# Performance work log

Hardware: AMD Instinct MI355X
Metric: run time of the kernel (lower is better)

Reference implementation:

```python
import jax, jax.numpy as jnp
import numpy as np

LMAX, MMAX = 4, 2
C = 128          # sphere_channels
MOUT = 128       # m_output_channels
N = 32768        # number of edges
K = sum(2 * min(l, MMAX) + 1 for l in range(LMAX + 1))  # 19 coefficients
LN_EPS = 1e-5


def build_to_m():
    # l-major ordering of (l, m) coefficients -> m-major permutation matrix
    ms = np.array([m for l in range(LMAX + 1)
                   for m in range(-min(l, MMAX), min(l, MMAX) + 1)])
    order = list(np.nonzero(ms == 0)[0])
    for m in range(1, MMAX + 1):
        order += list(np.nonzero(ms == m)[0]) + list(np.nonzero(ms == -m)[0])
    P = np.zeros((K, K), np.float32)
    P[np.arange(K), order] = 1.0
    return jnp.asarray(P)


TO_M = build_to_m()
M_SIZE = [LMAX + 1] + [LMAX - m + 1 for m in range(1, MMAX + 1)]  # [5, 4, 3]


def _layernorm(h, g, b):
    mu = jnp.mean(h, axis=-1, keepdims=True)
    var = jnp.mean(jnp.square(h - mu), axis=-1, keepdims=True)
    return (h - mu) * jax.lax.rsqrt(var + LN_EPS) * g + b


def _radial_mlp(x, w1, b1, g1, be1, w2, b2, g2, be2, w3, b3):
    h = jax.nn.silu(_layernorm(x @ w1.T + b1, g1, be1))
    h = jax.nn.silu(_layernorm(h @ w2.T + b2, g2, be2))
    return h @ w3.T + b3  # [N, 1536]


def setup_inputs() -> dict:
    key = jax.random.key(0)
    ks = jax.random.split(key, 16)
    s = 0.02
    return {
        "x": jax.random.normal(ks[0], (N, K, C), jnp.float32),
        "x_edge": jax.random.normal(ks[1], (N, C), jnp.float32),
        "fc0_w": jax.random.normal(ks[2], (MOUT * 5, 5 * C), jnp.float32) * s,
        "fc0_b": jax.random.normal(ks[3], (MOUT * 5,), jnp.float32) * s,
        "fc1_w": jax.random.normal(ks[4], (MOUT * 4, 4 * C), jnp.float32) * s,
        "fc2_w": jax.random.normal(ks[5], (MOUT * 3, 3 * C), jnp.float32) * s,
        "rad_w1": jax.random.normal(ks[6], (C, C), jnp.float32) * s,
        "rad_b1": jax.random.normal(ks[7], (C,), jnp.float32) * s,
        "rad_g1": jnp.ones((C,), jnp.float32),
        "rad_beta1": jnp.zeros((C,), jnp.float32),
        "rad_w2": jax.random.normal(ks[8], (C, C), jnp.float32) * s,
        "rad_b2": jax.random.normal(ks[9], (C,), jnp.float32) * s,
        "rad_g2": jnp.ones((C,), jnp.float32),
        "rad_beta2": jnp.zeros((C,), jnp.float32),
        "rad_w3": jax.random.normal(ks[10], (1536, C), jnp.float32) * s,
        "rad_b3": jax.random.normal(ks[11], (1536,), jnp.float32) * s,
    }


def reference(x, x_edge, fc0_w, fc0_b, fc1_w, fc2_w,
              rad_w1, rad_b1, rad_g1, rad_beta1,
              rad_w2, rad_b2, rad_g2, rad_beta2,
              rad_w3, rad_b3):
    n = x.shape[0]
    # reorder coefficients by m (to_m is a permutation)
    xm = jnp.einsum('nac,ba->nbc', x, TO_M)
    rad = _radial_mlp(x_edge, rad_w1, rad_b1, rad_g1, rad_beta1,
                      rad_w2, rad_b2, rad_g2, rad_beta2, rad_w3, rad_b3)

    # m = 0 block
    sz0 = M_SIZE[0]
    x0 = xm[:, :sz0].reshape(n, sz0 * C) * rad[:, :sz0 * C]
    y0 = (x0 @ fc0_w.T + fc0_b).reshape(n, sz0, MOUT)
    outs = [y0]

    offset, offr = sz0, sz0 * C
    for m, fcw in zip((1, 2), (fc1_w, fc2_w)):
        sz = M_SIZE[m]
        din = sz * C
        xb = xm[:, offset:offset + 2 * sz].reshape(n, 2, din)
        xb = xb * rad[:, offr:offr + din][:, None, :]  # FiLM radial scale
        yb = (xb @ fcw.T).reshape(n, 2 * sz, MOUT)
        outs.append(yb)
        offset += 2 * sz
        offr += din

    out = jnp.concatenate(outs, axis=1)  # [N, K, MOUT]
    # project back from m-major ordering
    return jnp.einsum('nac,ab->nbc', out, TO_M)
```

## Files before the change

### kernel.cpp

```cpp
#include <hip/hip_runtime.h>

typedef __bf16 bf16x8 __attribute__((ext_vector_type(8)));
typedef __bf16 bf16x4 __attribute__((ext_vector_type(4)));
typedef float f32x4 __attribute__((ext_vector_type(4)));

#define MFMA_16x16x32_BF16(a, b, c) __builtin_amdgcn_mfma_f32_16x16x32_bf16(a, b, c, 0, 0, 0)

typedef const __attribute__((address_space(1))) unsigned int* gas_ptr;
typedef __attribute__((address_space(3))) unsigned int* las_ptr;

__device__ __forceinline__ void gload_lds16(const void* g, void* l) {
    __builtin_amdgcn_global_load_lds((gas_ptr)(unsigned long long)g,
                                     (las_ptr)(unsigned long long)l, 16, 0, 0);
}

__constant__ int ORDER_C[19] = {0, 2, 6, 11, 16, 3, 7, 12, 17, 1, 5, 10, 15, 8, 13, 18, 4, 9, 14};

__global__ __launch_bounds__(256) void wconv_kernel(
    const float* __restrict__ fc0, const float* __restrict__ fc1,
    const float* __restrict__ fc2, const float* __restrict__ rw1,
    const float* __restrict__ rw2, const float* __restrict__ rw3,
    __bf16* __restrict__ o) {
    int i4 = (blockIdx.x * 256 + threadIdx.x) * 4;
    const float* s;
    int rel;
    if (i4 < 409600)      { s = fc0; rel = i4; }
    else if (i4 < 671744) { s = fc1; rel = i4 - 409600; }
    else if (i4 < 819200) { s = fc2; rel = i4 - 671744; }
    else if (i4 < 835584) { s = rw1; rel = i4 - 819200; }
    else if (i4 < 851968) { s = rw2; rel = i4 - 835584; }
    else                  { s = rw3; rel = i4 - 851968; }
    float4 v = *(const float4*)(s + rel);
    bf16x4 b;
    b[0] = (__bf16)v.x; b[1] = (__bf16)v.y; b[2] = (__bf16)v.z; b[3] = (__bf16)v.w;
    *(bf16x4*)(o + i4) = b;
}

__global__ __launch_bounds__(256) void xconv_kernel(const float* __restrict__ xe,
                                                    __bf16* __restrict__ o) {
    int i4 = (blockIdx.x * 256 + threadIdx.x) * 4;
    float4 v = *(const float4*)(xe + i4);
    bf16x4 b;
    b[0] = (__bf16)v.x; b[1] = (__bf16)v.y; b[2] = (__bf16)v.z; b[3] = (__bf16)v.w;
    *(bf16x4*)(o + i4) = b;
}

__global__ __launch_bounds__(256) void gemm128_kernel(const __bf16* __restrict__ Ain,
                                                      const __bf16* __restrict__ Wb,
                                                      float* __restrict__ outp) {
    __shared__ __align__(16) __bf16 As[128 * 128];
    __shared__ __align__(16) __bf16 Bs[128 * 128];
    const int tid = threadIdx.x;
    const int w = tid >> 6, lane = tid & 63;
    const int quad = lane >> 4, l16 = lane & 15;
    const int e0 = blockIdx.x * 128;

    {
        const char* ga = (const char*)(Ain + (size_t)e0 * 128);
        const char* gb = (const char*)Wb;
        for (int r = 0; r < 8; ++r) {
            int boff = (r * 4 + w) * 1024 + lane * 16;
            gload_lds16(ga + boff, (char*)As + boff);
            gload_lds16(gb + boff, (char*)Bs + boff);
        }
    }
    __syncthreads();

    const int wr = w >> 1, wc = w & 1;
    f32x4 acc[4][4] = {};
    for (int ks = 0; ks < 4; ++ks) {
        bf16x8 af[4], bfr[4];
        for (int i = 0; i < 4; ++i)
            af[i] = *(const bf16x8*)&As[(wr * 64 + i * 16 + l16) * 128 + ks * 32 + quad * 8];
        for (int j = 0; j < 4; ++j)
            bfr[j] = *(const bf16x8*)&Bs[(wc * 64 + j * 16 + l16) * 128 + ks * 32 + quad * 8];
        for (int i = 0; i < 4; ++i)
            for (int j = 0; j < 4; ++j)
                acc[i][j] = MFMA_16x16x32_BF16(af[i], bfr[j], acc[i][j]);
    }

    for (int i = 0; i < 4; ++i)
        for (int j = 0; j < 4; ++j) {
            const int col = wc * 64 + j * 16 + l16;
            for (int r = 0; r < 4; ++r) {
                const int row = e0 + wr * 64 + i * 16 + quad * 4 + r;
                outp[(size_t)row * 128 + col] = acc[i][j][r];
            }
        }
}

__global__ __launch_bounds__(256) void lnsilu_kernel(const float* __restrict__ hp,
                                                     const float* __restrict__ bvec,
                                                     const float* __restrict__ g,
                                                     const float* __restrict__ be,
                                                     __bf16* __restrict__ hs) {
    const int tid = threadIdx.x;
    const int w = tid >> 6, lane = tid & 63;
    const int row = blockIdx.x * 4 + w;
    const float* hr = hp + (size_t)row * 128;
    float a = hr[lane] + bvec[lane];
    float b = hr[lane + 64] + bvec[lane + 64];
    float s = a + b;
    s += __shfl_xor(s, 1);  s += __shfl_xor(s, 2);  s += __shfl_xor(s, 4);
    s += __shfl_xor(s, 8);  s += __shfl_xor(s, 16); s += __shfl_xor(s, 32);
    const float mu = s * (1.f / 128.f);
    const float da = a - mu, db = b - mu;
    float v = da * da + db * db;
    v += __shfl_xor(v, 1);  v += __shfl_xor(v, 2);  v += __shfl_xor(v, 4);
    v += __shfl_xor(v, 8);  v += __shfl_xor(v, 16); v += __shfl_xor(v, 32);
    const float rs = rsqrtf(v * (1.f / 128.f) + 1e-5f);
    float ya = da * rs * g[lane] + be[lane];
    float yb = db * rs * g[lane + 64] + be[lane + 64];
    ya = ya / (1.f + __expf(-ya));
    yb = yb / (1.f + __expf(-yb));
    hs[(size_t)row * 128 + lane] = (__bf16)ya;
    hs[(size_t)row * 128 + lane + 64] = (__bf16)yb;
}

__global__ __launch_bounds__(256) void radial3_kernel(
    const __bf16* __restrict__ h2g, const __bf16* __restrict__ w3b,
    const float* __restrict__ b3, __bf16* __restrict__ radg) {
    __shared__ __align__(16) __bf16 As[128 * 128];
    __shared__ __align__(16) __bf16 Bs[128 * 128];
    const int tid = threadIdx.x;
    const int w = tid >> 6, lane = tid & 63;
    const int quad = lane >> 4, l16 = lane & 15;
    const int e0 = blockIdx.x * 128, n0 = blockIdx.y * 128;

    {
        const char* ga = (const char*)(h2g + (size_t)e0 * 128);
        const char* gb = (const char*)(w3b + (size_t)n0 * 128);
        for (int r = 0; r < 8; ++r) {
            int boff = (r * 4 + w) * 1024 + lane * 16;
            gload_lds16(ga + boff, (char*)As + boff);
            gload_lds16(gb + boff, (char*)Bs + boff);
        }
    }
    __syncthreads();

    const int wr = w >> 1, wc = w & 1;
    f32x4 acc[4][4] = {};
    for (int ks = 0; ks < 4; ++ks) {
        bf16x8 af[4], bfr[4];
        for (int i = 0; i < 4; ++i)
            af[i] = *(const bf16x8*)&As[(wr * 64 + i * 16 + l16) * 128 + ks * 32 + quad * 8];
        for (int j = 0; j < 4; ++j)
            bfr[j] = *(const bf16x8*)&Bs[(wc * 64 + j * 16 + l16) * 128 + ks * 32 + quad * 8];
        for (int i = 0; i < 4; ++i)
            for (int j = 0; j < 4; ++j)
                acc[i][j] = MFMA_16x16x32_BF16(af[i], bfr[j], acc[i][j]);
    }
    __syncthreads();

    float bcol[4];
    for (int j = 0; j < 4; ++j) bcol[j] = b3[n0 + wc * 64 + j * 16 + l16];
    for (int i = 0; i < 4; ++i)
        for (int j = 0; j < 4; ++j)
            for (int r = 0; r < 4; ++r) {
                int row = wr * 64 + i * 16 + quad * 4 + r;
                int col = wc * 64 + j * 16 + l16;
                As[row * 128 + col] = (__bf16)(acc[i][j][r] + bcol[j]);
            }
    __syncthreads();
    for (int r = 0; r < 8; ++r) {
        int idx = r * 256 + tid;
        int e = idx >> 4, c = (idx & 15) * 8;
        *(uint4*)(radg + (size_t)(e0 + e) * 1536 + n0 + c) = *(const uint4*)&As[e * 128 + c];
    }
}

__global__ __launch_bounds__(256) void so2_main_kernel(
    const float* __restrict__ xg, const __bf16* __restrict__ radg,
    const __bf16* __restrict__ wfc0, const __bf16* __restrict__ wfc1,
    const __bf16* __restrict__ wfc2, const float* __restrict__ fc0b,
    float* __restrict__ outg) {
    __shared__ __align__(16) __bf16 As[128 * 64];
    __shared__ __align__(16) __bf16 Bs[128 * 64];
    const int tid = threadIdx.x;
    const int w = tid >> 6, lane = tid & 63;
    const int quad = lane >> 4, l16 = lane & 15;
    const int e0 = blockIdx.x * 128;
    const int y = blockIdx.y;

    int bstart, sz, rado, K;
    const __bf16* W;
    if (y < 5)       { bstart = 0;  sz = 5; rado = 0;    W = wfc0; K = 640; }
    else if (y < 9)  { bstart = 5;  sz = 4; rado = 640;  W = wfc1; K = 512; }
    else if (y < 13) { bstart = 9;  sz = 4; rado = 640;  W = wfc1; K = 512; }
    else if (y < 16) { bstart = 13; sz = 3; rado = 1152; W = wfc2; K = 384; }
    else             { bstart = 16; sz = 3; rado = 1152; W = wfc2; K = 384; }
    const int s_out = y - bstart;
    const int outrow = ORDER_C[y];
    const int wr = w >> 1, wc = w & 1;

    f32x4 acc[4][4] = {};

    const int e_ = tid >> 4;
    const int cA = (tid & 15) * 4;
    const char* wbase = (const char*)W + ((size_t)s_out * 128 * K) * 2;

    const int nkt = sz * 2;
    for (int kt = 0; kt < nkt; ++kt) {
        const int s_in = kt >> 1, cb = (kt & 1) * 64;
        const int xrow = ORDER_C[bstart + s_in];
        {
            const float* xp = xg + (size_t)(e0 + e_) * 2432 + xrow * 128 + cb + cA;
            const __bf16* rp = radg + (size_t)(e0 + e_) * 1536 + rado + s_in * 128 + cb + cA;
            for (int r = 0; r < 8; ++r) {
                float4 xv = *(const float4*)(xp + (size_t)r * 16 * 2432);
                bf16x4 rv = *(const bf16x4*)(rp + (size_t)r * 16 * 1536);
                bf16x4 av;
                av[0] = (__bf16)(xv.x * (float)rv[0]);
                av[1] = (__bf16)(xv.y * (float)rv[1]);
                av[2] = (__bf16)(xv.z * (float)rv[2]);
                av[3] = (__bf16)(xv.w * (float)rv[3]);
                *(bf16x4*)&As[(e_ + r * 16) * 64 + cA] = av;
            }
        }
        {
            const char* wkt = wbase + (size_t)kt * 128;
            for (int r = 0; r < 4; ++r) {
                int boff = (r * 4 + w) * 1024 + lane * 16;
                int col = boff >> 7, kb = boff & 127;
                gload_lds16(wkt + (size_t)col * K * 2 + kb, (char*)Bs + boff);
            }
        }
        __syncthreads();
        for (int ks = 0; ks < 2; ++ks) {
            bf16x8 af[4], bfr[4];
            for (int i = 0; i < 4; ++i)
                af[i] = *(const bf16x8*)&As[(wr * 64 + i * 16 + l16) * 64 + ks * 32 + quad * 8];
            for (int j = 0; j < 4; ++j)
                bfr[j] = *(const bf16x8*)&Bs[(wc * 64 + j * 16 + l16) * 64 + ks * 32 + quad * 8];
            for (int i = 0; i < 4; ++i)
                for (int j = 0; j < 4; ++j)
                    acc[i][j] = MFMA_16x16x32_BF16(af[i], bfr[j], acc[i][j]);
        }
        __syncthreads();
    }

    float bv[4];
    for (int j = 0; j < 4; ++j)
        bv[j] = (y < 5) ? fc0b[s_out * 128 + wc * 64 + j * 16 + l16] : 0.f;
    for (int i = 0; i < 4; ++i)
        for (int j = 0; j < 4; ++j) {
            const int col = wc * 64 + j * 16 + l16;
            for (int r = 0; r < 4; ++r) {
                const int row = e0 + wr * 64 + i * 16 + quad * 4 + r;
                outg[(size_t)row * 2432 + outrow * 128 + col] = acc[i][j][r] + bv[j];
            }
        }
}

extern "C" void kernel_launch(void* const* d_in, const int* in_sizes, int n_in,
                              void* d_out, int out_size, void* d_ws, size_t ws_size,
                              hipStream_t stream) {
    const float* x       = (const float*)d_in[0];
    const float* x_edge  = (const float*)d_in[1];
    const float* fc0_w   = (const float*)d_in[2];
    const float* fc0_b   = (const float*)d_in[3];
    const float* fc1_w   = (const float*)d_in[4];
    const float* fc2_w   = (const float*)d_in[5];
    const float* rad_w1  = (const float*)d_in[6];
    const float* rad_b1  = (const float*)d_in[7];
    const float* rad_g1  = (const float*)d_in[8];
    const float* rad_be1 = (const float*)d_in[9];
    const float* rad_w2  = (const float*)d_in[10];
    const float* rad_b2  = (const float*)d_in[11];
    const float* rad_g2  = (const float*)d_in[12];
    const float* rad_be2 = (const float*)d_in[13];
    const float* rad_w3  = (const float*)d_in[14];
    const float* rad_b3  = (const float*)d_in[15];
    float* out = (float*)d_out;

    const int N = in_sizes[0] / (19 * 128);

    __bf16* wb  = (__bf16*)d_ws;
    __bf16* sh  = (__bf16*)((char*)d_ws + (2u << 20));
    char*   rb  = (char*)d_ws + (10u << 20);
    float*  hp  = (float*)rb;
    __bf16* rad = (__bf16*)rb;
    __bf16* wfc0 = wb;
    __bf16* wfc1 = wb + 409600;
    __bf16* wfc2 = wb + 671744;
    __bf16* w1b  = wb + 819200;
    __bf16* w2b  = wb + 835584;
    __bf16* w3b  = wb + 851968;

    wconv_kernel<<<dim3(1024), dim3(256), 0, stream>>>(fc0_w, fc1_w, fc2_w, rad_w1, rad_w2,
                                                       rad_w3, wb);
    xconv_kernel<<<dim3(4096), dim3(256), 0, stream>>>(x_edge, sh);
    gemm128_kernel<<<dim3(N / 128), dim3(256), 0, stream>>>(sh, w1b, hp);
    lnsilu_kernel<<<dim3(N / 4), dim3(256), 0, stream>>>(hp, rad_b1, rad_g1, rad_be1, sh);
    gemm128_kernel<<<dim3(N / 128), dim3(256), 0, stream>>>(sh, w2b, hp);
    lnsilu_kernel<<<dim3(N / 4), dim3(256), 0, stream>>>(hp, rad_b2, rad_g2, rad_be2, sh);
    radial3_kernel<<<dim3(N / 128, 12), dim3(256), 0, stream>>>(sh, w3b, rad_b3, rad);
    so2_main_kernel<<<dim3(N / 128, 19), dim3(256), 0, stream>>>(x, rad, wfc0, wfc1, wfc2,
                                                                 fc0_b, out);
}
```

Baseline: 804.6 us.

## Fuse radial GEMM with LayerNorm-SiLU, swizzle LDS, merge conversions, regroup SO2 blocks

```diff
diff --git a/kernel.cpp b/kernel.cpp
--- a/kernel.cpp
+++ b/kernel.cpp
@@ -16,40 +16,43 @@
 
 __constant__ int ORDER_C[19] = {0, 2, 6, 11, 16, 3, 7, 12, 17, 1, 5, 10, 15, 8, 13, 18, 4, 9, 14};
 
-__global__ __launch_bounds__(256) void wconv_kernel(
+__global__ __launch_bounds__(256) void wxconv_kernel(
     const float* __restrict__ fc0, const float* __restrict__ fc1,
     const float* __restrict__ fc2, const float* __restrict__ rw1,
     const float* __restrict__ rw2, const float* __restrict__ rw3,
-    __bf16* __restrict__ o) {
-    int i4 = (blockIdx.x * 256 + threadIdx.x) * 4;
+    const float* __restrict__ xe, __bf16* __restrict__ wo,
+    __bf16* __restrict__ xo) {
+    const int bid = blockIdx.x;
     const float* s;
-    int rel;
-    if (i4 < 409600)      { s = fc0; rel = i4; }
-    else if (i4 < 671744) { s = fc1; rel = i4 - 409600; }
-    else if (i4 < 819200) { s = fc2; rel = i4 - 671744; }
-    else if (i4 < 835584) { s = rw1; rel = i4 - 819200; }
-    else if (i4 < 851968) { s = rw2; rel = i4 - 835584; }
-    else                  { s = rw3; rel = i4 - 851968; }
+    __bf16* o;
+    int i4, rel;
+    if (bid < 1024) {
+        i4 = (bid * 256 + threadIdx.x) * 4;
+        o = wo;
+        if (i4 < 409600)      { s = fc0; rel = i4; }
+        else if (i4 < 671744) { s = fc1; rel = i4 - 409600; }
+        else if (i4 < 819200) { s = fc2; rel = i4 - 671744; }
+        else if (i4 < 835584) { s = rw1; rel = i4 - 819200; }
+        else if (i4 < 851968) { s = rw2; rel = i4 - 835584; }
+        else                  { s = rw3; rel = i4 - 851968; }
+    } else {
+        i4 = ((bid - 1024) * 256 + threadIdx.x) * 4;
+        o = xo; s = xe; rel = i4;
+    }
     float4 v = *(const float4*)(s + rel);
     bf16x4 b;
     b[0] = (__bf16)v.x; b[1] = (__bf16)v.y; b[2] = (__bf16)v.z; b[3] = (__bf16)v.w;
     *(bf16x4*)(o + i4) = b;
 }
 
-__global__ __launch_bounds__(256) void xconv_kernel(const float* __restrict__ xe,
-                                                    __bf16* __restrict__ o) {
-    int i4 = (blockIdx.x * 256 + threadIdx.x) * 4;
-    float4 v = *(const float4*)(xe + i4);
-    bf16x4 b;
-    b[0] = (__bf16)v.x; b[1] = (__bf16)v.y; b[2] = (__bf16)v.z; b[3] = (__bf16)v.w;
-    *(bf16x4*)(o + i4) = b;
-}
-
-__global__ __launch_bounds__(256) void gemm128_kernel(const __bf16* __restrict__ Ain,
-                                                      const __bf16* __restrict__ Wb,
-                                                      float* __restrict__ outp) {
-    __shared__ __align__(16) __bf16 As[128 * 128];
-    __shared__ __align__(16) __bf16 Bs[128 * 128];
+__global__ __launch_bounds__(256) void gemmln_kernel(
+    const __bf16* __restrict__ Ain, const __bf16* __restrict__ Wb,
+    const float* __restrict__ bvec, const float* __restrict__ gv,
+    const float* __restrict__ bev, __bf16* __restrict__ hs) {
+    __shared__ __align__(16) char smem[65536];
+    __bf16* As = (__bf16*)smem;
+    __bf16* Bs = (__bf16*)(smem + 32768);
+    float*  Fs = (float*)smem;
     const int tid = threadIdx.x;
     const int w = tid >> 6, lane = tid & 63;
     const int quad = lane >> 4, l16 = lane & 15;
@@ -60,8 +63,9 @@
         const char* gb = (const char*)Wb;
         for (int r = 0; r < 8; ++r) {
             int boff = (r * 4 + w) * 1024 + lane * 16;
-            gload_lds16(ga + boff, (char*)As + boff);
-            gload_lds16(gb + boff, (char*)Bs + boff);
+            int soff = boff ^ (((boff >> 8) & 15) << 4);
+            gload_lds16(ga + soff, (char*)As + boff);
+            gload_lds16(gb + soff, (char*)Bs + boff);
         }
     }
     __syncthreads();
@@ -70,51 +74,51 @@
     f32x4 acc[4][4] = {};
     for (int ks = 0; ks < 4; ++ks) {
         bf16x8 af[4], bfr[4];
-        for (int i = 0; i < 4; ++i)
-            af[i] = *(const bf16x8*)&As[(wr * 64 + i * 16 + l16) * 128 + ks * 32 + quad * 8];
-        for (int j = 0; j < 4; ++j)
-            bfr[j] = *(const bf16x8*)&Bs[(wc * 64 + j * 16 + l16) * 128 + ks * 32 + quad * 8];
+        for (int i = 0; i < 4; ++i) {
+            int ar = wr * 64 + i * 16 + l16;
+            af[i] = *(const bf16x8*)&As[ar * 128 + ((ks * 32 + quad * 8) ^ ((ar & 15) << 3))];
+        }
+        for (int j = 0; j < 4; ++j) {
+            int br = wc * 64 + j * 16 + l16;
+            bfr[j] = *(const bf16x8*)&Bs[br * 128 + ((ks * 32 + quad * 8) ^ ((br & 15) << 3))];
+        }
         for (int i = 0; i < 4; ++i)
             for (int j = 0; j < 4; ++j)
                 acc[i][j] = MFMA_16x16x32_BF16(af[i], bfr[j], acc[i][j]);
     }
-
+    __syncthreads();
+
+    float bc[4];
+    for (int j = 0; j < 4; ++j) bc[j] = bvec[wc * 64 + j * 16 + l16];
     for (int i = 0; i < 4; ++i)
-        for (int j = 0; j < 4; ++j) {
-            const int col = wc * 64 + j * 16 + l16;
-            for (int r = 0; r < 4; ++r) {
-                const int row = e0 + wr * 64 + i * 16 + quad * 4 + r;
-                outp[(size_t)row * 128 + col] = acc[i][j][r];
-            }
-        }
-}
-
-__global__ __launch_bounds__(256) void lnsilu_kernel(const float* __restrict__ hp,
-                                                     const float* __restrict__ bvec,
-                                                     const float* __restrict__ g,
-                                                     const float* __restrict__ be,
-                                                     __bf16* __restrict__ hs) {
-    const int tid = threadIdx.x;
-    const int w = tid >> 6, lane = tid & 63;
-    const int row = blockIdx.x * 4 + w;
-    const float* hr = hp + (size_t)row * 128;
-    float a = hr[lane] + bvec[lane];
-    float b = hr[lane + 64] + bvec[lane + 64];
-    float s = a + b;
-    s += __shfl_xor(s, 1);  s += __shfl_xor(s, 2);  s += __shfl_xor(s, 4);
-    s += __shfl_xor(s, 8);  s += __shfl_xor(s, 16); s += __shfl_xor(s, 32);
-    const float mu = s * (1.f / 128.f);
-    const float da = a - mu, db = b - mu;
-    float v = da * da + db * db;
-    v += __shfl_xor(v, 1);  v += __shfl_xor(v, 2);  v += __shfl_xor(v, 4);
-    v += __shfl_xor(v, 8);  v += __shfl_xor(v, 16); v += __shfl_xor(v, 32);
-    const float rs = rsqrtf(v * (1.f / 128.f) + 1e-5f);
-    float ya = da * rs * g[lane] + be[lane];
-    float yb = db * rs * g[lane + 64] + be[lane + 64];
-    ya = ya / (1.f + __expf(-ya));
-    yb = yb / (1.f + __expf(-yb));
-    hs[(size_t)row * 128 + lane] = (__bf16)ya;
-    hs[(size_t)row * 128 + lane + 64] = (__bf16)yb;
+        for (int j = 0; j < 4; ++j)
+            for (int r = 0; r < 4; ++r)
+                Fs[(wr * 64 + i * 16 + quad * 4 + r) * 128 + wc * 64 + j * 16 + l16] =
+                    acc[i][j][r] + bc[j];
+    __syncthreads();
+
+    const float gl = gv[lane], gh = gv[lane + 64];
+    const float bl = bev[lane], bh = bev[lane + 64];
+    for (int it = 0; it < 32; ++it) {
+        const int row = it * 4 + w;
+        float a = Fs[row * 128 + lane];
+        float b = Fs[row * 128 + lane + 64];
+        float s = a + b;
+        s += __shfl_xor(s, 1);  s += __shfl_xor(s, 2);  s += __shfl_xor(s, 4);
+        s += __shfl_xor(s, 8);  s += __shfl_xor(s, 16); s += __shfl_xor(s, 32);
+        const float mu = s * (1.f / 128.f);
+        const float da = a - mu, db = b - mu;
+        float v = da * da + db * db;
+        v += __shfl_xor(v, 1);  v += __shfl_xor(v, 2);  v += __shfl_xor(v, 4);
+        v += __shfl_xor(v, 8);  v += __shfl_xor(v, 16); v += __shfl_xor(v, 32);
+        const float rs = rsqrtf(v * (1.f / 128.f) + 1e-5f);
+        float ya = da * rs * gl + bl;
+        float yb = db * rs * gh + bh;
+        ya = ya / (1.f + __expf(-ya));
+        yb = yb / (1.f + __expf(-yb));
+        hs[(size_t)(e0 + row) * 128 + lane] = (__bf16)ya;
+        hs[(size_t)(e0 + row) * 128 + lane + 64] = (__bf16)yb;
+    }
 }
 
 __global__ __launch_bounds__(256) void radial3_kernel(
@@ -132,8 +136,9 @@
         const char* gb = (const char*)(w3b + (size_t)n0 * 128);
         for (int r = 0; r < 8; ++r) {
             int boff = (r * 4 + w) * 1024 + lane * 16;
-            gload_lds16(ga + boff, (char*)As + boff);
-            gload_lds16(gb + boff, (char*)Bs + boff);
+            int soff = boff ^ (((boff >> 8) & 15) << 4);
+            gload_lds16(ga + soff, (char*)As + boff);
+            gload_lds16(gb + soff, (char*)Bs + boff);
         }
     }
     __syncthreads();
@@ -142,10 +147,14 @@
     f32x4 acc[4][4] = {};
     for (int ks = 0; ks < 4; ++ks) {
         bf16x8 af[4], bfr[4];
-        for (int i = 0; i < 4; ++i)
-            af[i] = *(const bf16x8*)&As[(wr * 64 + i * 16 + l16) * 128 + ks * 32 + quad * 8];
-        for (int j = 0; j < 4; ++j)
-            bfr[j] = *(const bf16x8*)&Bs[(wc * 64 + j * 16 + l16) * 128 + ks * 32 + quad * 8];
+        for (int i = 0; i < 4; ++i) {
+            int ar = wr * 64 + i * 16 + l16;
+            af[i] = *(const bf16x8*)&As[ar * 128 + ((ks * 32 + quad * 8) ^ ((ar & 15) << 3))];
+        }
+        for (int j = 0; j < 4; ++j) {
+            int br = wc * 64 + j * 16 + l16;
+            bfr[j] = *(const bf16x8*)&Bs[br * 128 + ((ks * 32 + quad * 8) ^ ((br & 15) << 3))];
+        }
         for (int i = 0; i < 4; ++i)
             for (int j = 0; j < 4; ++j)
                 acc[i][j] = MFMA_16x16x32_BF16(af[i], bfr[j], acc[i][j]);
@@ -180,76 +189,80 @@
     const int w = tid >> 6, lane = tid & 63;
     const int quad = lane >> 4, l16 = lane & 15;
     const int e0 = blockIdx.x * 128;
-    const int y = blockIdx.y;
-
-    int bstart, sz, rado, K;
-    const __bf16* W;
-    if (y < 5)       { bstart = 0;  sz = 5; rado = 0;    W = wfc0; K = 640; }
-    else if (y < 9)  { bstart = 5;  sz = 4; rado = 640;  W = wfc1; K = 512; }
-    else if (y < 13) { bstart = 9;  sz = 4; rado = 640;  W = wfc1; K = 512; }
-    else if (y < 16) { bstart = 13; sz = 3; rado = 1152; W = wfc2; K = 384; }
-    else             { bstart = 16; sz = 3; rado = 1152; W = wfc2; K = 384; }
-    const int s_out = y - bstart;
-    const int outrow = ORDER_C[y];
+    const int gid = blockIdx.y;
+
+    const int bstart = (gid == 0) ? 0 : (gid == 1) ? 5 : (gid == 2) ? 9 : (gid == 3) ? 13 : 16;
+    const int sz     = (gid == 0) ? 5 : (gid < 3) ? 4 : 3;
+    const int rado   = (gid == 0) ? 0 : (gid < 3) ? 640 : 1152;
+    const int K      = sz * 128;
+    const __bf16* W  = (gid == 0) ? wfc0 : (gid < 3) ? wfc1 : wfc2;
+
     const int wr = w >> 1, wc = w & 1;
-
-    f32x4 acc[4][4] = {};
-
     const int e_ = tid >> 4;
     const int cA = (tid & 15) * 4;
-    const char* wbase = (const char*)W + ((size_t)s_out * 128 * K) * 2;
-
-    const int nkt = sz * 2;
-    for (int kt = 0; kt < nkt; ++kt) {
-        const int s_in = kt >> 1, cb = (kt & 1) * 64;
-        const int xrow = ORDER_C[bstart + s_in];
-        {
-            const float* xp = xg + (size_t)(e0 + e_) * 2432 + xrow * 128 + cb + cA;
-            const __bf16* rp = radg + (size_t)(e0 + e_) * 1536 + rado + s_in * 128 + cb + cA;
-            for (int r = 0; r < 8; ++r) {
-                float4 xv = *(const float4*)(xp + (size_t)r * 16 * 2432);
-                bf16x4 rv = *(const bf16x4*)(rp + (size_t)r * 16 * 1536);
-                bf16x4 av;
-                av[0] = (__bf16)(xv.x * (float)rv[0]);
-                av[1] = (__bf16)(xv.y * (float)rv[1]);
-                av[2] = (__bf16)(xv.z * (float)rv[2]);
-                av[3] = (__bf16)(xv.w * (float)rv[3]);
-                *(bf16x4*)&As[(e_ + r * 16) * 64 + cA] = av;
-            }
-        }
-        {
-            const char* wkt = wbase + (size_t)kt * 128;
-            for (int r = 0; r < 4; ++r) {
-                int boff = (r * 4 + w) * 1024 + lane * 16;
-                int col = boff >> 7, kb = boff & 127;
-                gload_lds16(wkt + (size_t)col * K * 2 + kb, (char*)Bs + boff);
-            }
-        }
-        __syncthreads();
-        for (int ks = 0; ks < 2; ++ks) {
-            bf16x8 af[4], bfr[4];
-            for (int i = 0; i < 4; ++i)
-                af[i] = *(const bf16x8*)&As[(wr * 64 + i * 16 + l16) * 64 + ks * 32 + quad * 8];
-            for (int j = 0; j < 4; ++j)
-                bfr[j] = *(const bf16x8*)&Bs[(wc * 64 + j * 16 + l16) * 64 + ks * 32 + quad * 8];
-            for (int i = 0; i < 4; ++i)
-                for (int j = 0; j < 4; ++j)
-                    acc[i][j] = MFMA_16x16x32_BF16(af[i], bfr[j], acc[i][j]);
-        }
-        __syncthreads();
-    }
-
-    float bv[4];
-    for (int j = 0; j < 4; ++j)
-        bv[j] = (y < 5) ? fc0b[s_out * 128 + wc * 64 + j * 16 + l16] : 0.f;
-    for (int i = 0; i < 4; ++i)
-        for (int j = 0; j < 4; ++j) {
-            const int col = wc * 64 + j * 16 + l16;
-            for (int r = 0; r < 4; ++r) {
-                const int row = e0 + wr * 64 + i * 16 + quad * 4 + r;
-                outg[(size_t)row * 2432 + outrow * 128 + col] = acc[i][j][r] + bv[j];
-            }
-        }
+
+    for (int so = 0; so < sz; ++so) {
+        f32x4 acc[4][4] = {};
+        const char* wbase = (const char*)W + ((size_t)so * 128 * K) * 2;
+        const int nkt = 2 * sz;
+        for (int kt = 0; kt < nkt; ++kt) {
+            const int s_in = kt >> 1, cb = (kt & 1) * 64;
+            const int xrow = ORDER_C[bstart + s_in];
+            {
+                const float* xp = xg + (size_t)(e0 + e_) * 2432 + xrow * 128 + cb + cA;
+                const __bf16* rp = radg + (size_t)(e0 + e_) * 1536 + rado + s_in * 128 + cb + cA;
+                for (int r = 0; r < 8; ++r) {
+                    float4 xv = *(const float4*)(xp + (size_t)r * 16 * 2432);
+                    bf16x4 rv = *(const bf16x4*)(rp + (size_t)r * 16 * 1536);
+                    bf16x4 av;
+                    av[0] = (__bf16)(xv.x * (float)rv[0]);
+                    av[1] = (__bf16)(xv.y * (float)rv[1]);
+                    av[2] = (__bf16)(xv.z * (float)rv[2]);
+                    av[3] = (__bf16)(xv.w * (float)rv[3]);
+                    const int arow = e_ + r * 16;
+                    *(bf16x4*)&As[arow * 64 + (cA ^ ((arow & 7) << 3))] = av;
+                }
+            }
+            {
+                const char* wkt = wbase + (size_t)kt * 128;
+                for (int r = 0; r < 4; ++r) {
+                    int boff = (r * 4 + w) * 1024 + lane * 16;
+                    int col = boff >> 7, kb = boff & 127;
+                    gload_lds16(wkt + (size_t)col * K * 2 + (kb ^ ((col & 7) << 4)),
+                                (char*)Bs + boff);
+                }
+            }
+            __syncthreads();
+            for (int ks = 0; ks < 2; ++ks) {
+                bf16x8 af[4], bfr[4];
+                for (int i = 0; i < 4; ++i) {
+                    int ar = wr * 64 + i * 16 + l16;
+                    af[i] = *(const bf16x8*)&As[ar * 64 + ((ks * 32 + quad * 8) ^ ((ar & 7) << 3))];
+                }
+                for (int j = 0; j < 4; ++j) {
+                    int br = wc * 64 + j * 16 + l16;
+                    bfr[j] = *(const bf16x8*)&Bs[br * 64 + ((ks * 32 + quad * 8) ^ ((br & 7) << 3))];
+                }
+                for (int i = 0; i < 4; ++i)
+                    for (int j = 0; j < 4; ++j)
+                        acc[i][j] = MFMA_16x16x32_BF16(af[i], bfr[j], acc[i][j]);
+            }
+            __syncthreads();
+        }
+
+        const int outrow = ORDER_C[bstart + so];
+        float bv[4];
+        for (int j = 0; j < 4; ++j)
+            bv[j] = (gid == 0) ? fc0b[so * 128 + wc * 64 + j * 16 + l16] : 0.f;
+        for (int i = 0; i < 4; ++i)
+            for (int j = 0; j < 4; ++j) {
+                const int col = wc * 64 + j * 16 + l16;
+                for (int r = 0; r < 4; ++r) {
+                    const int row = e0 + wr * 64 + i * 16 + quad * 4 + r;
+                    outg[(size_t)row * 2432 + outrow * 128 + col] = acc[i][j][r] + bv[j];
+                }
+            }
+    }
 }
 
 extern "C" void kernel_launch(void* const* d_in, const int* in_sizes, int n_in,
@@ -277,9 +290,9 @@
 
     __bf16* wb  = (__bf16*)d_ws;
     __bf16* sh  = (__bf16*)((char*)d_ws + (2u << 20));
-    char*   rb  = (char*)d_ws + (10u << 20);
-    float*  hp  = (float*)rb;
-    __bf16* rad = (__bf16*)rb;
+    __bf16* rb  = (__bf16*)((char*)d_ws + (10u << 20));
+    __bf16* h1  = rb;
+    __bf16* rad = rb;
     __bf16* wfc0 = wb;
     __bf16* wfc1 = wb + 409600;
     __bf16* wfc2 = wb + 671744;
@@ -287,14 +300,13 @@
     __bf16* w2b  = wb + 835584;
     __bf16* w3b  = wb + 851968;
 
-    wconv_kernel<<<dim3(1024), dim3(256), 0, stream>>>(fc0_w, fc1_w, fc2_w, rad_w1, rad_w2,
-                                                       rad_w3, wb);
-    xconv_kernel<<<dim3(4096), dim3(256), 0, stream>>>(x_edge, sh);
-    gemm128_kernel<<<dim3(N / 128), dim3(256), 0, stream>>>(sh, w1b, hp);
-    lnsilu_kernel<<<dim3(N / 4), dim3(256), 0, stream>>>(hp, rad_b1, rad_g1, rad_be1, sh);
-    gemm128_kernel<<<dim3(N / 128), dim3(256), 0, stream>>>(sh, w2b, hp);
-    lnsilu_kernel<<<dim3(N / 4), dim3(256), 0, stream>>>(hp, rad_b2, rad_g2, rad_be2, sh);
+    wxconv_kernel<<<dim3(5120), dim3(256), 0, stream>>>(fc0_w, fc1_w, fc2_w, rad_w1,
+                                                        rad_w2, rad_w3, x_edge, wb, sh);
+    gemmln_kernel<<<dim3(N / 128), dim3(256), 0, stream>>>(sh, w1b, rad_b1, rad_g1,
+                                                           rad_be1, h1);
+    gemmln_kernel<<<dim3(N / 128), dim3(256), 0, stream>>>(h1, w2b, rad_b2, rad_g2,
+                                                           rad_be2, sh);
     radial3_kernel<<<dim3(N / 128, 12), dim3(256), 0, stream>>>(sh, w3b, rad_b3, rad);
-    so2_main_kernel<<<dim3(N / 128, 19), dim3(256), 0, stream>>>(x, rad, wfc0, wfc1, wfc2,
-                                                                 fc0_b, out);
-}
+    so2_main_kernel<<<dim3(N / 128, 5), dim3(256), 0, stream>>>(x, rad, wfc0, wfc1, wfc2,
+                                                                fc0_b, out);
+}
```

New measurement: 857.1 us. 1.07x slower.
